# Kernel optimization log

Hardware: AMD Instinct MI355X
Metric: run time of the kernel (lower is better)

Reference implementation:

```python
import jax, jax.numpy as jnp
import numpy as np

B, H, S, D = 2, 16, 2048, 64

def setup_inputs() -> dict:
    key = jax.random.key(0)
    kq, kk, kv = jax.random.split(key, 3)
    q = jax.random.normal(kq, (B, H, S, D), dtype=jnp.float32)
    k = jax.random.normal(kk, (B, H, S, D), dtype=jnp.float32)
    v = jax.random.normal(kv, (B, H, S, D), dtype=jnp.float32)
    # causal mask, True = attend
    mask = jnp.broadcast_to(jnp.tril(jnp.ones((S, S), dtype=bool)), (B, H, S, S))
    return {"q": q, "k": k, "v": v, "mask": mask}

def reference(q, k, v, mask):
    dim = q.shape[-1]
    scale = 1.0 / jnp.sqrt(jnp.asarray(dim, q.dtype))
    scores = jnp.einsum('bhqd,bhkd->bhqk', q, k) * scale  # [B,H,S,S]
    scores = jnp.where(mask, scores, jnp.finfo(scores.dtype).min)
    probs = jax.nn.softmax(scores, axis=-1)
    return jnp.einsum('bhqk,bhkd->bhqd', probs, v)
```

## Files before the change

kernel.cpp:

```cpp
#include <hip/hip_runtime.h>

#define B_   2
#define H_   16
#define S_   2048
#define D_   64
#define BQ   128
#define BK   64
#define NW   8
#define QSCALE 0.18033688011112042f
#define DEFER_THR 8.0f

typedef _Float16 f16x8 __attribute__((ext_vector_type(8)));
typedef _Float16 f16x4 __attribute__((ext_vector_type(4)));
typedef float    f32x4 __attribute__((ext_vector_type(4)));

typedef const unsigned int __attribute__((address_space(1))) gu32;
typedef unsigned int       __attribute__((address_space(3))) lu32;

#define KBYTES_PER_HEAD (S_ * 128)
#define WS_V_OFF ((size_t)B_ * H_ * KBYTES_PER_HEAD)
#define WS_NEED  (2 * WS_V_OFF)

__global__ __launch_bounds__(256) void prep_kv(const float* __restrict__ K,
                                               const float* __restrict__ V,
                                               char* __restrict__ ws)
{
    if (blockIdx.x < (B_ * H_ * S_ * 8) / 256) {
        const int gidx = blockIdx.x * 256 + threadIdx.x;
        const int gcol = gidx & 7;
        const int srow = gidx >> 3;
        const float4* src = (const float4*)(K + (size_t)srow * D_ + gcol * 8);
        float4 a = src[0], b = src[1];
        f16x8 h;
        h[0] = (_Float16)a.x; h[1] = (_Float16)a.y; h[2] = (_Float16)a.z; h[3] = (_Float16)a.w;
        h[4] = (_Float16)b.x; h[5] = (_Float16)b.y; h[6] = (_Float16)b.z; h[7] = (_Float16)b.w;
        const int s  = srow & (S_ - 1);
        const int bh = srow >> 11;
        size_t off = (size_t)bh * KBYTES_PER_HEAD + (size_t)(s >> 6) * 8192
                   + (s & 63) * 128 + ((gcol ^ (s & 7)) << 4);
        *(f16x8*)(ws + off) = h;
    } else {
        __shared__ _Float16 Vl[64][72];
        const int tile = blockIdx.x - (B_ * H_ * S_ * 8) / 256;
        const int bh = tile >> 5, t = tile & 31;
        const float* vb = V + ((size_t)bh * S_ + t * 64) * D_;
        const int tid = threadIdx.x;
        #pragma unroll
        for (int it = 0; it < 2; ++it) {
            const int row = (tid >> 3) + it * 32;
            const int c8  = (tid & 7) * 8;
            const float4* p = (const float4*)(vb + row * D_ + c8);
            float4 a = p[0], b = p[1];
            f16x8 h;
            h[0] = (_Float16)a.x; h[1] = (_Float16)a.y; h[2] = (_Float16)a.z; h[3] = (_Float16)a.w;
            h[4] = (_Float16)b.x; h[5] = (_Float16)b.y; h[6] = (_Float16)b.z; h[7] = (_Float16)b.w;
            *(f16x8*)&Vl[row][c8] = h;
        }
        __syncthreads();
        char* out = ws + WS_V_OFF + (size_t)bh * KBYTES_PER_HEAD + t * 8192;
        #pragma unroll
        for (int it = 0; it < 2; ++it) {
            const int task = tid + it * 256;
            const int d = task >> 3, kg = task & 7;
            f16x8 h;
            #pragma unroll
            for (int j = 0; j < 8; ++j) h[j] = Vl[kg * 8 + j][d];
            *(f16x8*)(out + d * 128 + ((kg ^ (d & 7)) << 4)) = h;
        }
    }
}

template<bool MASK>
__device__ __forceinline__ void compute_tile(
    const _Float16* __restrict__ SMb, _Float16 (*__restrict__ Plw)[72],
    const f16x8 aq[2], f32x4 accO[4], float& m_r, float& l_r,
    int g, int l15, int sx, int dq)
{
    const _Float16* Kb = SMb;
    const _Float16* Vb = SMb + 4096;

    f32x4 accS[4];
    #pragma unroll
    for (int s = 0; s < 4; ++s) accS[s] = (f32x4){0.f, 0.f, 0.f, 0.f};
    __builtin_amdgcn_s_setprio(1);
    #pragma unroll
    for (int sub = 0; sub < 4; ++sub) {
        if (MASK && (sub * 16 > dq + 15)) continue;
        #pragma unroll
        for (int kc = 0; kc < 2; ++kc) {
            f16x8 ak = *(const f16x8*)(Kb + ((sub * 16 + l15) * 64 + (((kc * 4 + g) ^ sx) << 3)));
            accS[sub] = __builtin_amdgcn_mfma_f32_16x16x32_f16(ak, aq[kc], accS[sub], 0, 0, 0);
        }
    }
    __builtin_amdgcn_s_setprio(0);

    float ps[4][4];
    float pmax = -1e30f;
    #pragma unroll
    for (int sub = 0; sub < 4; ++sub) {
        const bool fullmask = MASK && (sub * 16 > dq + 15);
        const bool diag     = MASK && !fullmask && (sub * 16 + 15 > dq);
        #pragma unroll
        for (int r = 0; r < 4; ++r) {
            float s = fullmask ? -1e30f : accS[sub][r];
            if (diag && (sub * 16 + g * 4 + r > dq + l15)) s = -1e30f;
            ps[sub][r] = s;
            pmax = fmaxf(pmax, s);
        }
    }

    if (!__all(pmax <= m_r + DEFER_THR)) {
        float mx = pmax;
        mx = fmaxf(mx, __shfl_xor(mx, 16));
        mx = fmaxf(mx, __shfl_xor(mx, 32));
        const float mnew  = fmaxf(m_r, mx);
        const float alpha = __builtin_amdgcn_exp2f(m_r - mnew);
        l_r *= alpha;
        #pragma unroll
        for (int d = 0; d < 4; ++d)
            #pragma unroll
            for (int r = 0; r < 4; ++r) accO[d][r] *= alpha;
        m_r = mnew;
    }

    #pragma unroll
    for (int sub = 0; sub < 4; ++sub)
        #pragma unroll
        for (int r = 0; r < 4; ++r)
            ps[sub][r] = __builtin_amdgcn_exp2f(ps[sub][r] - m_r);

    #pragma unroll
    for (int sub = 0; sub < 4; ++sub) {
        f16x4 q4;
        q4[0] = (_Float16)ps[sub][0]; q4[1] = (_Float16)ps[sub][1];
        q4[2] = (_Float16)ps[sub][2]; q4[3] = (_Float16)ps[sub][3];
        *(f16x4*)&Plw[l15][sub * 16 + g * 4] = q4;
    }

    float rs = 0.f;
    #pragma unroll
    for (int sub = 0; sub < 4; ++sub)
        #pragma unroll
        for (int r = 0; r < 4; ++r) rs += ps[sub][r];
    l_r += rs;

    asm volatile("s_waitcnt lgkmcnt(0)" ::: "memory");
    __builtin_amdgcn_sched_barrier(0);

    f16x8 pb[2];
    pb[0] = *(const f16x8*)&Plw[l15][g * 8];
    pb[1] = *(const f16x8*)&Plw[l15][32 + g * 8];

    __builtin_amdgcn_s_setprio(1);
    #pragma unroll
    for (int d = 0; d < 4; ++d)
        #pragma unroll
        for (int kc = 0; kc < 2; ++kc) {
            f16x8 av = *(const f16x8*)(Vb + ((d * 16 + l15) * 64 + (((kc * 4 + g) ^ sx) << 3)));
            accO[d] = __builtin_amdgcn_mfma_f32_16x16x32_f16(av, pb[kc], accO[d], 0, 0, 0);
        }
    __builtin_amdgcn_s_setprio(0);
}

__global__ __launch_bounds__(512, 4) void attn_main(
    const float* __restrict__ Q, const char* __restrict__ ws, float* __restrict__ O)
{
    __shared__ _Float16 SM[2][8192];
    __shared__ _Float16 Pl[NW][16][72];

    const int tid  = threadIdx.x;
    const int lane = tid & 63;
    const int w    = tid >> 6;
    const int g    = lane >> 4;
    const int l15  = lane & 15;
    const int sx   = l15 & 7;

    const int id    = blockIdx.x;
    const int bh    = id & 31;
    const int qi    = id >> 5;
    const int qt    = (id < 256) ? (15 - qi) : (qi - 8);
    const int qbase = qt * BQ;

    const char* kbase = ws + (size_t)bh * KBYTES_PER_HEAD;
    const char* vbase = ws + WS_V_OFF + (size_t)bh * KBYTES_PER_HEAD;

    f16x8 aq[2];
    {
        const float* qrow = Q + ((size_t)bh * S_ + qbase + w * 16 + l15) * D_;
        #pragma unroll
        for (int kc = 0; kc < 2; ++kc) {
            const float4* p = (const float4*)(qrow + kc * 32 + g * 8);
            float4 x0 = p[0], x1 = p[1];
            f16x8 h;
            h[0] = (_Float16)(x0.x * QSCALE); h[1] = (_Float16)(x0.y * QSCALE);
            h[2] = (_Float16)(x0.z * QSCALE); h[3] = (_Float16)(x0.w * QSCALE);
            h[4] = (_Float16)(x1.x * QSCALE); h[5] = (_Float16)(x1.y * QSCALE);
            h[6] = (_Float16)(x1.z * QSCALE); h[7] = (_Float16)(x1.w * QSCALE);
            aq[kc] = h;
        }
    }

    f32x4 accO[4];
    #pragma unroll
    for (int i = 0; i < 4; ++i) accO[i] = (f32x4){0.f, 0.f, 0.f, 0.f};
    float m_r = -1e30f, l_r = 0.f;

    const int nt = 2 * qt + 2;
    const int dqw = qbase + w * 16;

    auto STAGE = [&](int t, int buf) {
        #pragma unroll
        for (int i = 0; i < 2; ++i) {
            const int c = w * 2 + i;
            const char* src = (c < 8 ? kbase + (size_t)t * 8192 + c * 1024
                                     : vbase + (size_t)t * 8192 + (c - 8) * 1024) + lane * 16;
            __builtin_amdgcn_global_load_lds((gu32*)src, (lu32*)&SM[buf][c * 512], 16, 0, 0);
        }
    };

    STAGE(0, 0);
    for (int t = 0; t < nt - 2; ++t) {
        STAGE(t + 1, (t + 1) & 1);
        asm volatile("s_waitcnt vmcnt(2)" ::: "memory");
        __builtin_amdgcn_s_barrier();
        compute_tile<false>(&SM[t & 1][0], Pl[w], aq, accO, m_r, l_r, g, l15, sx, 0);
        __builtin_amdgcn_s_barrier();
    }
    STAGE(nt - 1, (nt - 1) & 1);
    asm volatile("s_waitcnt vmcnt(2)" ::: "memory");
    __builtin_amdgcn_s_barrier();
    compute_tile<true>(&SM[(nt - 2) & 1][0], Pl[w], aq, accO, m_r, l_r, g, l15, sx,
                       dqw - (nt - 2) * 64);
    __builtin_amdgcn_s_barrier();
    asm volatile("s_waitcnt vmcnt(0)" ::: "memory");
    __builtin_amdgcn_s_barrier();
    compute_tile<true>(&SM[(nt - 1) & 1][0], Pl[w], aq, accO, m_r, l_r, g, l15, sx,
                       dqw - (nt - 1) * 64);

    float l = l_r;
    l += __shfl_xor(l, 16);
    l += __shfl_xor(l, 32);
    const float inv = 1.0f / l;
    float* orow = O + ((size_t)bh * S_ + qbase + w * 16 + l15) * D_;
    #pragma unroll
    for (int d = 0; d < 4; ++d) {
        f32x4 o = accO[d] * inv;
        *(f32x4*)&orow[d * 16 + g * 4] = o;
    }
}

extern "C" void kernel_launch(void* const* d_in, const int* in_sizes, int n_in,
                              void* d_out, int out_size, void* d_ws, size_t ws_size,
                              hipStream_t stream) {
    const float* q = (const float*)d_in[0];
    const float* k = (const float*)d_in[1];
    const float* v = (const float*)d_in[2];
    float* o = (float*)d_out;
    char* ws = (char*)d_ws;

    if (ws_size < WS_NEED) return;

    const int kblocks = (B_ * H_ * S_ * 8) / 256;
    const int vblocks = B_ * H_ * (S_ / 64);
    prep_kv<<<kblocks + vblocks, 256, 0, stream>>>(k, v, ws);
    attn_main<<<(S_ / BQ) * B_ * H_, 512, 0, stream>>>(q, ws, o);
}
```

Measured before the change: 53.52 us.

## Process two 16-row query slabs per wave with four waves per block

```diff
diff --git a/kernel.cpp b/kernel.cpp
--- a/kernel.cpp
+++ b/kernel.cpp
@@ -6,12 +6,12 @@
 #define D_   64
 #define BQ   128
 #define BK   64
-#define NW   8
+#define NW   4
 #define QSCALE 0.18033688011112042f
 #define DEFER_THR 8.0f
 
+typedef _Float16 f16x4 __attribute__((ext_vector_type(4)));
 typedef _Float16 f16x8 __attribute__((ext_vector_type(8)));
-typedef _Float16 f16x4 __attribute__((ext_vector_type(4)));
 typedef float    f32x4 __attribute__((ext_vector_type(4)));
 
 typedef const unsigned int __attribute__((address_space(1))) gu32;
@@ -72,84 +72,93 @@
 
 template<bool MASK>
 __device__ __forceinline__ void compute_tile(
-    const _Float16* __restrict__ SMb, _Float16 (*__restrict__ Plw)[72],
-    const f16x8 aq[2], f32x4 accO[4], float& m_r, float& l_r,
-    int g, int l15, int sx, int dq)
+    const _Float16* __restrict__ SMb, _Float16 (*__restrict__ Plw)[16][72],
+    const f16x8 aq[2][2], f32x4 accO[2][4], float m_r[2], float l_r[2],
+    int g, int l15, int sx, int dqw)
 {
     const _Float16* Kb = SMb;
     const _Float16* Vb = SMb + 4096;
 
-    f32x4 accS[4];
-    #pragma unroll
-    for (int s = 0; s < 4; ++s) accS[s] = (f32x4){0.f, 0.f, 0.f, 0.f};
+    f32x4 accS[2][4];
+    #pragma unroll
+    for (int qs = 0; qs < 2; ++qs)
+        #pragma unroll
+        for (int s = 0; s < 4; ++s) accS[qs][s] = (f32x4){0.f, 0.f, 0.f, 0.f};
+
     __builtin_amdgcn_s_setprio(1);
     #pragma unroll
     for (int sub = 0; sub < 4; ++sub) {
-        if (MASK && (sub * 16 > dq + 15)) continue;
+        if (MASK && (sub * 16 > dqw + 31)) continue;
         #pragma unroll
         for (int kc = 0; kc < 2; ++kc) {
             f16x8 ak = *(const f16x8*)(Kb + ((sub * 16 + l15) * 64 + (((kc * 4 + g) ^ sx) << 3)));
-            accS[sub] = __builtin_amdgcn_mfma_f32_16x16x32_f16(ak, aq[kc], accS[sub], 0, 0, 0);
+            accS[0][sub] = __builtin_amdgcn_mfma_f32_16x16x32_f16(ak, aq[0][kc], accS[0][sub], 0, 0, 0);
+            accS[1][sub] = __builtin_amdgcn_mfma_f32_16x16x32_f16(ak, aq[1][kc], accS[1][sub], 0, 0, 0);
         }
     }
     __builtin_amdgcn_s_setprio(0);
 
-    float ps[4][4];
-    float pmax = -1e30f;
-    #pragma unroll
-    for (int sub = 0; sub < 4; ++sub) {
-        const bool fullmask = MASK && (sub * 16 > dq + 15);
-        const bool diag     = MASK && !fullmask && (sub * 16 + 15 > dq);
-        #pragma unroll
-        for (int r = 0; r < 4; ++r) {
-            float s = fullmask ? -1e30f : accS[sub][r];
-            if (diag && (sub * 16 + g * 4 + r > dq + l15)) s = -1e30f;
-            ps[sub][r] = s;
-            pmax = fmaxf(pmax, s);
-        }
-    }
-
-    if (!__all(pmax <= m_r + DEFER_THR)) {
-        float mx = pmax;
-        mx = fmaxf(mx, __shfl_xor(mx, 16));
-        mx = fmaxf(mx, __shfl_xor(mx, 32));
-        const float mnew  = fmaxf(m_r, mx);
-        const float alpha = __builtin_amdgcn_exp2f(m_r - mnew);
-        l_r *= alpha;
-        #pragma unroll
-        for (int d = 0; d < 4; ++d)
-            #pragma unroll
-            for (int r = 0; r < 4; ++r) accO[d][r] *= alpha;
-        m_r = mnew;
-    }
-
-    #pragma unroll
-    for (int sub = 0; sub < 4; ++sub)
-        #pragma unroll
-        for (int r = 0; r < 4; ++r)
-            ps[sub][r] = __builtin_amdgcn_exp2f(ps[sub][r] - m_r);
-
-    #pragma unroll
-    for (int sub = 0; sub < 4; ++sub) {
-        f16x4 q4;
-        q4[0] = (_Float16)ps[sub][0]; q4[1] = (_Float16)ps[sub][1];
-        q4[2] = (_Float16)ps[sub][2]; q4[3] = (_Float16)ps[sub][3];
-        *(f16x4*)&Plw[l15][sub * 16 + g * 4] = q4;
-    }
-
-    float rs = 0.f;
-    #pragma unroll
-    for (int sub = 0; sub < 4; ++sub)
-        #pragma unroll
-        for (int r = 0; r < 4; ++r) rs += ps[sub][r];
-    l_r += rs;
+    #pragma unroll
+    for (int qs = 0; qs < 2; ++qs) {
+        const int dqb = dqw + qs * 16;
+        float ps[4][4];
+        float pmax = -1e30f;
+        #pragma unroll
+        for (int sub = 0; sub < 4; ++sub) {
+            const bool fullmask = MASK && (sub * 16 > dqb + 15);
+            const bool diag     = MASK && !fullmask && (sub * 16 + 15 > dqb);
+            #pragma unroll
+            for (int r = 0; r < 4; ++r) {
+                float s = fullmask ? -1e30f : accS[qs][sub][r];
+                if (diag && (sub * 16 + g * 4 + r > dqb + l15)) s = -1e30f;
+                ps[sub][r] = s;
+                pmax = fmaxf(pmax, s);
+            }
+        }
+
+        if (!__all(pmax <= m_r[qs] + DEFER_THR)) {
+            float mx = pmax;
+            mx = fmaxf(mx, __shfl_xor(mx, 16));
+            mx = fmaxf(mx, __shfl_xor(mx, 32));
+            const float mnew  = fmaxf(m_r[qs], mx);
+            const float alpha = __builtin_amdgcn_exp2f(m_r[qs] - mnew);
+            l_r[qs] *= alpha;
+            #pragma unroll
+            for (int d = 0; d < 4; ++d)
+                #pragma unroll
+                for (int r = 0; r < 4; ++r) accO[qs][d][r] *= alpha;
+            m_r[qs] = mnew;
+        }
+
+        float rs = 0.f;
+        #pragma unroll
+        for (int sub = 0; sub < 4; ++sub)
+            #pragma unroll
+            for (int r = 0; r < 4; ++r) {
+                const float p = __builtin_amdgcn_exp2f(ps[sub][r] - m_r[qs]);
+                ps[sub][r] = p;
+                rs += p;
+            }
+        l_r[qs] += rs;
+
+        #pragma unroll
+        for (int sub = 0; sub < 4; ++sub) {
+            f16x4 q4;
+            q4[0] = (_Float16)ps[sub][0]; q4[1] = (_Float16)ps[sub][1];
+            q4[2] = (_Float16)ps[sub][2]; q4[3] = (_Float16)ps[sub][3];
+            *(f16x4*)&Plw[qs][l15][sub * 16 + g * 4] = q4;
+        }
+    }
 
     asm volatile("s_waitcnt lgkmcnt(0)" ::: "memory");
     __builtin_amdgcn_sched_barrier(0);
 
-    f16x8 pb[2];
-    pb[0] = *(const f16x8*)&Plw[l15][g * 8];
-    pb[1] = *(const f16x8*)&Plw[l15][32 + g * 8];
+    f16x8 pb[2][2];
+    #pragma unroll
+    for (int qs = 0; qs < 2; ++qs) {
+        pb[qs][0] = *(const f16x8*)&Plw[qs][l15][g * 8];
+        pb[qs][1] = *(const f16x8*)&Plw[qs][l15][32 + g * 8];
+    }
 
     __builtin_amdgcn_s_setprio(1);
     #pragma unroll
@@ -157,16 +166,17 @@
         #pragma unroll
         for (int kc = 0; kc < 2; ++kc) {
             f16x8 av = *(const f16x8*)(Vb + ((d * 16 + l15) * 64 + (((kc * 4 + g) ^ sx) << 3)));
-            accO[d] = __builtin_amdgcn_mfma_f32_16x16x32_f16(av, pb[kc], accO[d], 0, 0, 0);
+            accO[0][d] = __builtin_amdgcn_mfma_f32_16x16x32_f16(av, pb[0][kc], accO[0][d], 0, 0, 0);
+            accO[1][d] = __builtin_amdgcn_mfma_f32_16x16x32_f16(av, pb[1][kc], accO[1][d], 0, 0, 0);
         }
     __builtin_amdgcn_s_setprio(0);
 }
 
-__global__ __launch_bounds__(512, 4) void attn_main(
+__global__ __launch_bounds__(256, 2) void attn_main(
     const float* __restrict__ Q, const char* __restrict__ ws, float* __restrict__ O)
 {
     __shared__ _Float16 SM[2][8192];
-    __shared__ _Float16 Pl[NW][16][72];
+    __shared__ _Float16 Pl[NW][2][16][72];
 
     const int tid  = threadIdx.x;
     const int lane = tid & 63;
@@ -184,9 +194,10 @@
     const char* kbase = ws + (size_t)bh * KBYTES_PER_HEAD;
     const char* vbase = ws + WS_V_OFF + (size_t)bh * KBYTES_PER_HEAD;
 
-    f16x8 aq[2];
-    {
-        const float* qrow = Q + ((size_t)bh * S_ + qbase + w * 16 + l15) * D_;
+    f16x8 aq[2][2];
+    #pragma unroll
+    for (int qs = 0; qs < 2; ++qs) {
+        const float* qrow = Q + ((size_t)bh * S_ + qbase + w * 32 + qs * 16 + l15) * D_;
         #pragma unroll
         for (int kc = 0; kc < 2; ++kc) {
             const float4* p = (const float4*)(qrow + kc * 32 + g * 8);
@@ -196,22 +207,24 @@
             h[2] = (_Float16)(x0.z * QSCALE); h[3] = (_Float16)(x0.w * QSCALE);
             h[4] = (_Float16)(x1.x * QSCALE); h[5] = (_Float16)(x1.y * QSCALE);
             h[6] = (_Float16)(x1.z * QSCALE); h[7] = (_Float16)(x1.w * QSCALE);
-            aq[kc] = h;
-        }
-    }
-
-    f32x4 accO[4];
-    #pragma unroll
-    for (int i = 0; i < 4; ++i) accO[i] = (f32x4){0.f, 0.f, 0.f, 0.f};
-    float m_r = -1e30f, l_r = 0.f;
+            aq[qs][kc] = h;
+        }
+    }
+
+    f32x4 accO[2][4];
+    #pragma unroll
+    for (int qs = 0; qs < 2; ++qs)
+        #pragma unroll
+        for (int i = 0; i < 4; ++i) accO[qs][i] = (f32x4){0.f, 0.f, 0.f, 0.f};
+    float m_r[2] = {-1e30f, -1e30f};
+    float l_r[2] = {0.f, 0.f};
 
     const int nt = 2 * qt + 2;
-    const int dqw = qbase + w * 16;
 
     auto STAGE = [&](int t, int buf) {
         #pragma unroll
-        for (int i = 0; i < 2; ++i) {
-            const int c = w * 2 + i;
+        for (int i = 0; i < 4; ++i) {
+            const int c = w * 4 + i;
             const char* src = (c < 8 ? kbase + (size_t)t * 8192 + c * 1024
                                      : vbase + (size_t)t * 8192 + (c - 8) * 1024) + lane * 16;
             __builtin_amdgcn_global_load_lds((gu32*)src, (lu32*)&SM[buf][c * 512], 16, 0, 0);
@@ -221,31 +234,34 @@
     STAGE(0, 0);
     for (int t = 0; t < nt - 2; ++t) {
         STAGE(t + 1, (t + 1) & 1);
-        asm volatile("s_waitcnt vmcnt(2)" ::: "memory");
+        asm volatile("s_waitcnt vmcnt(4)" ::: "memory");
         __builtin_amdgcn_s_barrier();
         compute_tile<false>(&SM[t & 1][0], Pl[w], aq, accO, m_r, l_r, g, l15, sx, 0);
         __builtin_amdgcn_s_barrier();
     }
     STAGE(nt - 1, (nt - 1) & 1);
-    asm volatile("s_waitcnt vmcnt(2)" ::: "memory");
+    asm volatile("s_waitcnt vmcnt(4)" ::: "memory");
     __builtin_amdgcn_s_barrier();
     compute_tile<true>(&SM[(nt - 2) & 1][0], Pl[w], aq, accO, m_r, l_r, g, l15, sx,
-                       dqw - (nt - 2) * 64);
+                       qbase + w * 32 - (nt - 2) * 64);
     __builtin_amdgcn_s_barrier();
     asm volatile("s_waitcnt vmcnt(0)" ::: "memory");
     __builtin_amdgcn_s_barrier();
     compute_tile<true>(&SM[(nt - 1) & 1][0], Pl[w], aq, accO, m_r, l_r, g, l15, sx,
-                       dqw - (nt - 1) * 64);
-
-    float l = l_r;
-    l += __shfl_xor(l, 16);
-    l += __shfl_xor(l, 32);
-    const float inv = 1.0f / l;
-    float* orow = O + ((size_t)bh * S_ + qbase + w * 16 + l15) * D_;
-    #pragma unroll
-    for (int d = 0; d < 4; ++d) {
-        f32x4 o = accO[d] * inv;
-        *(f32x4*)&orow[d * 16 + g * 4] = o;
+                       qbase + w * 32 - (nt - 1) * 64);
+
+    #pragma unroll
+    for (int qs = 0; qs < 2; ++qs) {
+        float l = l_r[qs];
+        l += __shfl_xor(l, 16);
+        l += __shfl_xor(l, 32);
+        const float inv = 1.0f / l;
+        float* orow = O + ((size_t)bh * S_ + qbase + w * 32 + qs * 16 + l15) * D_;
+        #pragma unroll
+        for (int d = 0; d < 4; ++d) {
+            f32x4 o = accO[qs][d] * inv;
+            *(f32x4*)&orow[d * 16 + g * 4] = o;
+        }
     }
 }
 
@@ -263,5 +279,5 @@
     const int kblocks = (B_ * H_ * S_ * 8) / 256;
     const int vblocks = B_ * H_ * (S_ / 64);
     prep_kv<<<kblocks + vblocks, 256, 0, stream>>>(k, v, ws);
-    attn_main<<<(S_ / BQ) * B_ * H_, 512, 0, stream>>>(q, ws, o);
-}
+    attn_main<<<(S_ / BQ) * B_ * H_, 256, 0, stream>>>(q, ws, o);
+}
```

Result: slower. 59.58 us (+11.3%).

## Software-pipeline QK of next tile with softmax/PV of previous tile, triple-buffer LDS

Applied to the files above, without the earlier changes.

```diff
diff --git a/kernel.cpp b/kernel.cpp
--- a/kernel.cpp
+++ b/kernel.cpp
@@ -10,8 +10,8 @@
 #define QSCALE 0.18033688011112042f
 #define DEFER_THR 8.0f
 
+typedef _Float16 f16x4 __attribute__((ext_vector_type(4)));
 typedef _Float16 f16x8 __attribute__((ext_vector_type(8)));
-typedef _Float16 f16x4 __attribute__((ext_vector_type(4)));
 typedef float    f32x4 __attribute__((ext_vector_type(4)));
 
 typedef const unsigned int __attribute__((address_space(1))) gu32;
@@ -70,16 +70,12 @@
     }
 }
 
+
 template<bool MASK>
-__device__ __forceinline__ void compute_tile(
-    const _Float16* __restrict__ SMb, _Float16 (*__restrict__ Plw)[72],
-    const f16x8 aq[2], f32x4 accO[4], float& m_r, float& l_r,
+__device__ __forceinline__ void qk_tile(
+    const _Float16* __restrict__ Kb, const f16x8 aq[2], f32x4 (&accS)[4],
     int g, int l15, int sx, int dq)
 {
-    const _Float16* Kb = SMb;
-    const _Float16* Vb = SMb + 4096;
-
-    f32x4 accS[4];
     #pragma unroll
     for (int s = 0; s < 4; ++s) accS[s] = (f32x4){0.f, 0.f, 0.f, 0.f};
     __builtin_amdgcn_s_setprio(1);
@@ -93,21 +89,32 @@
         }
     }
     __builtin_amdgcn_s_setprio(0);
-
-    float ps[4][4];
+}
+
+template<bool MASK>
+__device__ __forceinline__ void smpv_tile(
+    const _Float16* __restrict__ SMb, _Float16 (*__restrict__ Plw)[72],
+    f32x4 (&accS)[4], f32x4 accO[4], float& m_r, float& l_r,
+    int g, int l15, int sx, int dq)
+{
+    const _Float16* Vb = SMb + 4096;
+
+    auto msk = [&](int sub, int r) -> float {
+        float s = accS[sub][r];
+        if (MASK) {
+            if (sub * 16 > dq + 15) s = -1e30f;
+            else if (sub * 16 + 15 > dq) {
+                if (sub * 16 + g * 4 + r > dq + l15) s = -1e30f;
+            }
+        }
+        return s;
+    };
+
     float pmax = -1e30f;
     #pragma unroll
-    for (int sub = 0; sub < 4; ++sub) {
-        const bool fullmask = MASK && (sub * 16 > dq + 15);
-        const bool diag     = MASK && !fullmask && (sub * 16 + 15 > dq);
-        #pragma unroll
-        for (int r = 0; r < 4; ++r) {
-            float s = fullmask ? -1e30f : accS[sub][r];
-            if (diag && (sub * 16 + g * 4 + r > dq + l15)) s = -1e30f;
-            ps[sub][r] = s;
-            pmax = fmaxf(pmax, s);
-        }
-    }
+    for (int sub = 0; sub < 4; ++sub)
+        #pragma unroll
+        for (int r = 0; r < 4; ++r) pmax = fmaxf(pmax, msk(sub, r));
 
     if (!__all(pmax <= m_r + DEFER_THR)) {
         float mx = pmax;
@@ -123,49 +130,42 @@
         m_r = mnew;
     }
 
-    #pragma unroll
-    for (int sub = 0; sub < 4; ++sub)
-        #pragma unroll
-        for (int r = 0; r < 4; ++r)
-            ps[sub][r] = __builtin_amdgcn_exp2f(ps[sub][r] - m_r);
-
+    float rs = 0.f;
     #pragma unroll
     for (int sub = 0; sub < 4; ++sub) {
+        float p0 = __builtin_amdgcn_exp2f(msk(sub, 0) - m_r);
+        float p1 = __builtin_amdgcn_exp2f(msk(sub, 1) - m_r);
+        float p2 = __builtin_amdgcn_exp2f(msk(sub, 2) - m_r);
+        float p3 = __builtin_amdgcn_exp2f(msk(sub, 3) - m_r);
+        rs += (p0 + p1) + (p2 + p3);
         f16x4 q4;
-        q4[0] = (_Float16)ps[sub][0]; q4[1] = (_Float16)ps[sub][1];
-        q4[2] = (_Float16)ps[sub][2]; q4[3] = (_Float16)ps[sub][3];
+        q4[0] = (_Float16)p0; q4[1] = (_Float16)p1;
+        q4[2] = (_Float16)p2; q4[3] = (_Float16)p3;
         *(f16x4*)&Plw[l15][sub * 16 + g * 4] = q4;
     }
-
-    float rs = 0.f;
-    #pragma unroll
-    for (int sub = 0; sub < 4; ++sub)
-        #pragma unroll
-        for (int r = 0; r < 4; ++r) rs += ps[sub][r];
     l_r += rs;
 
     asm volatile("s_waitcnt lgkmcnt(0)" ::: "memory");
     __builtin_amdgcn_sched_barrier(0);
 
-    f16x8 pb[2];
-    pb[0] = *(const f16x8*)&Plw[l15][g * 8];
-    pb[1] = *(const f16x8*)&Plw[l15][32 + g * 8];
+    f16x8 pb0 = *(const f16x8*)&Plw[l15][g * 8];
+    f16x8 pb1 = *(const f16x8*)&Plw[l15][32 + g * 8];
 
     __builtin_amdgcn_s_setprio(1);
     #pragma unroll
-    for (int d = 0; d < 4; ++d)
-        #pragma unroll
-        for (int kc = 0; kc < 2; ++kc) {
-            f16x8 av = *(const f16x8*)(Vb + ((d * 16 + l15) * 64 + (((kc * 4 + g) ^ sx) << 3)));
-            accO[d] = __builtin_amdgcn_mfma_f32_16x16x32_f16(av, pb[kc], accO[d], 0, 0, 0);
-        }
+    for (int d = 0; d < 4; ++d) {
+        f16x8 av0 = *(const f16x8*)(Vb + ((d * 16 + l15) * 64 + (((0 * 4 + g) ^ sx) << 3)));
+        accO[d] = __builtin_amdgcn_mfma_f32_16x16x32_f16(av0, pb0, accO[d], 0, 0, 0);
+        f16x8 av1 = *(const f16x8*)(Vb + ((d * 16 + l15) * 64 + (((1 * 4 + g) ^ sx) << 3)));
+        accO[d] = __builtin_amdgcn_mfma_f32_16x16x32_f16(av1, pb1, accO[d], 0, 0, 0);
+    }
     __builtin_amdgcn_s_setprio(0);
 }
 
 __global__ __launch_bounds__(512, 4) void attn_main(
     const float* __restrict__ Q, const char* __restrict__ ws, float* __restrict__ O)
 {
-    __shared__ _Float16 SM[2][8192];
+    __shared__ _Float16 SM[3][8192];
     __shared__ _Float16 Pl[NW][16][72];
 
     const int tid  = threadIdx.x;
@@ -204,38 +204,76 @@
     #pragma unroll
     for (int i = 0; i < 4; ++i) accO[i] = (f32x4){0.f, 0.f, 0.f, 0.f};
     float m_r = -1e30f, l_r = 0.f;
-
-    const int nt = 2 * qt + 2;
+    f32x4 accSA[4], accSB[4];
+
+    const int nt  = 2 * qt + 2;
     const int dqw = qbase + w * 16;
 
-    auto STAGE = [&](int t, int buf) {
+    _Float16* bQK = &SM[0][0];
+    _Float16* bST = &SM[1][0];
+    _Float16* bPV = &SM[2][0];
+
+    auto STAGE = [&](int t, _Float16* dst) {
         #pragma unroll
         for (int i = 0; i < 2; ++i) {
             const int c = w * 2 + i;
             const char* src = (c < 8 ? kbase + (size_t)t * 8192 + c * 1024
                                      : vbase + (size_t)t * 8192 + (c - 8) * 1024) + lane * 16;
-            __builtin_amdgcn_global_load_lds((gu32*)src, (lu32*)&SM[buf][c * 512], 16, 0, 0);
+            __builtin_amdgcn_global_load_lds((gu32*)src, (lu32*)(dst + c * 512), 16, 0, 0);
         }
     };
-
-    STAGE(0, 0);
-    for (int t = 0; t < nt - 2; ++t) {
-        STAGE(t + 1, (t + 1) & 1);
-        asm volatile("s_waitcnt vmcnt(2)" ::: "memory");
+    auto SYNC = []() {
+        asm volatile("s_waitcnt vmcnt(0)" ::: "memory");
         __builtin_amdgcn_s_barrier();
-        compute_tile<false>(&SM[t & 1][0], Pl[w], aq, accO, m_r, l_r, g, l15, sx, 0);
-        __builtin_amdgcn_s_barrier();
-    }
-    STAGE(nt - 1, (nt - 1) & 1);
-    asm volatile("s_waitcnt vmcnt(2)" ::: "memory");
-    __builtin_amdgcn_s_barrier();
-    compute_tile<true>(&SM[(nt - 2) & 1][0], Pl[w], aq, accO, m_r, l_r, g, l15, sx,
-                       dqw - (nt - 2) * 64);
-    __builtin_amdgcn_s_barrier();
-    asm volatile("s_waitcnt vmcnt(0)" ::: "memory");
-    __builtin_amdgcn_s_barrier();
-    compute_tile<true>(&SM[(nt - 1) & 1][0], Pl[w], aq, accO, m_r, l_r, g, l15, sx,
-                       dqw - (nt - 1) * 64);
+    };
+    auto ROT = [&]() { _Float16* tmp = bPV; bPV = bQK; bQK = bST; bST = tmp; };
+
+    STAGE(0, bQK);
+
+    SYNC();
+    STAGE(1, bST);
+    if (qt == 0) qk_tile<true >(bQK, aq, accSA, g, l15, sx, dqw);
+    else         qk_tile<false>(bQK, aq, accSA, g, l15, sx, 0);
+    ROT();
+
+    SYNC();
+    if (nt > 2) STAGE(2, bST);
+    if (qt == 0) {
+        qk_tile<true >(bQK, aq, accSB, g, l15, sx, dqw - 64);
+        smpv_tile<true >(bPV, Pl[w], accSA, accO, m_r, l_r, g, l15, sx, dqw);
+    } else {
+        qk_tile<false>(bQK, aq, accSB, g, l15, sx, 0);
+        smpv_tile<false>(bPV, Pl[w], accSA, accO, m_r, l_r, g, l15, sx, 0);
+    }
+    ROT();
+
+    for (int i = 1; i < qt; ++i) {
+        const int t0 = 2 * i;
+        SYNC();
+        STAGE(t0 + 1, bST);
+        qk_tile<false>(bQK, aq, accSA, g, l15, sx, 0);
+        smpv_tile<false>(bPV, Pl[w], accSB, accO, m_r, l_r, g, l15, sx, 0);
+        ROT();
+        SYNC();
+        STAGE(t0 + 2, bST);
+        qk_tile<false>(bQK, aq, accSB, g, l15, sx, 0);
+        smpv_tile<false>(bPV, Pl[w], accSA, accO, m_r, l_r, g, l15, sx, 0);
+        ROT();
+    }
+
+    if (qt >= 1) {
+        SYNC();
+        STAGE(nt - 1, bST);
+        qk_tile<true >(bQK, aq, accSA, g, l15, sx, dqw - (nt - 2) * 64);
+        smpv_tile<false>(bPV, Pl[w], accSB, accO, m_r, l_r, g, l15, sx, 0);
+        ROT();
+        SYNC();
+        qk_tile<true >(bQK, aq, accSB, g, l15, sx, dqw - (nt - 1) * 64);
+        smpv_tile<true >(bPV, Pl[w], accSA, accO, m_r, l_r, g, l15, sx, dqw - (nt - 2) * 64);
+        ROT();
+    }
+
+    smpv_tile<true>(bPV, Pl[w], accSB, accO, m_r, l_r, g, l15, sx, dqw - (nt - 1) * 64);
 
     float l = l_r;
     l += __shfl_xor(l, 16);
```

Result: faster. 50.93 us, median of 3 (-4.8%).
